# Kernel tuning notes

Measured on AMD Instinct MI355X. Metric: run time of the kernel, lower is better.

## Reference

```python
import jax, jax.numpy as jnp
import numpy as np

B, T, F, H = 256, 4096, 16, 64

def setup_inputs() -> dict:
    key = jax.random.key(0)
    ks = jax.random.split(key, 16)
    rn = lambda k, s, sc=0.1: jax.random.normal(k, s, dtype=jnp.float32) * sc
    return {
        'x':    rn(ks[0], (B, T, F), 1.0),
        'Wi1':  rn(ks[1], (F, 3 * H)), 'bi1': jnp.zeros((3 * H,), jnp.float32),
        'Whr1': rn(ks[2], (H, H)), 'Whz1': rn(ks[3], (H, H)), 'Whn1': rn(ks[4], (H, H)),
        'bhn1': jnp.zeros((H,), jnp.float32),
        'Wi2':  rn(ks[5], (H, 3 * H)), 'bi2': jnp.zeros((3 * H,), jnp.float32),
        'Whr2': rn(ks[6], (H, H)), 'Whz2': rn(ks[7], (H, H)), 'Whn2': rn(ks[8], (H, H)),
        'bhn2': jnp.zeros((H,), jnp.float32),
        'Wp':   rn(ks[9], (F, H)), 'bp': jnp.zeros((H,), jnp.float32),
        'Wa':   rn(ks[10], (H, 1)), 'ba': jnp.zeros((1,), jnp.float32),
        'W1':   rn(ks[11], (H, 128)), 'b1': jnp.zeros((128,), jnp.float32),
        'W2':   rn(ks[12], (128, 64)), 'b2': jnp.zeros((64,), jnp.float32),
        'W3':   rn(ks[13], (64, 32)), 'b3': jnp.zeros((32,), jnp.float32),
        'W4':   rn(ks[14], (32, 2)), 'b4': jnp.zeros((2,), jnp.float32),
    }

def gru_layer(x, Wi, bi, Whr, Whz, Whn, bhn):
    # flax GRUCell math: r/z hidden kernels bias-free; n hidden kernel has bias.
    b, h = x.shape[0], Whr.shape[0]
    xi = jnp.einsum('btf,fk->btk', x, Wi) + bi  # precompute input projections (B,T,3H)
    def step(hprev, xt):
        ir, iz, inn = jnp.split(xt, 3, axis=-1)
        r = jax.nn.sigmoid(ir + hprev @ Whr)
        z = jax.nn.sigmoid(iz + hprev @ Whz)
        n = jnp.tanh(inn + r * (hprev @ Whn + bhn))
        hnew = (1.0 - z) * n + z * hprev
        return hnew, hnew
    h0 = jnp.zeros((b, h), x.dtype)
    _, ys = jax.lax.scan(step, h0, jnp.swapaxes(xi, 0, 1))  # (T,B,H)
    return jnp.swapaxes(ys, 0, 1)  # (B,T,H)

def reference(x, Wi1, bi1, Whr1, Whz1, Whn1, bhn1,
              Wi2, bi2, Whr2, Whz2, Whn2, bhn2,
              Wp, bp, Wa, ba, W1, b1, W2, b2, W3, b3, W4, b4):
    o1 = gru_layer(x, Wi1, bi1, Whr1, Whz1, Whn1, bhn1)
    x_proj = jnp.einsum('btf,fh->bth', x, Wp) + bp  # F != H -> project
    o1 = o1 + 0.5 * x_proj
    o2 = gru_layer(o1, Wi2, bi2, Whr2, Whz2, Whn2, bhn2) + 0.5 * o1
    scores = jnp.einsum('bth,ho->bto', o2, Wa) + ba  # (B,T,1)
    w = jax.nn.softmax(scores, axis=1)
    attended = jnp.sum(o2 * w, axis=1)  # (B,H)
    h1 = jax.nn.relu(attended @ W1 + b1)
    h2 = jax.nn.relu(h1 @ W2 + b2)
    h3 = jax.nn.relu(h2 @ W3 + b3)
    return h3 @ W4 + b4  # (B,2)
```

## Files before the change

kernel.cpp:

```cpp
#include <hip/hip_runtime.h>


#define B_ 256
#define T_ 4096
#define F_ 16
#define H_ 64
#define L2E 1.4426950408889634f

typedef float v2f __attribute__((ext_vector_type(2)));

__device__ __forceinline__ float sigm(float x) {
    float e = __builtin_amdgcn_exp2f(-L2E * x);
    return __builtin_amdgcn_rcpf(1.0f + e);
}
__device__ __forceinline__ float tanh_(float x) {
    float e = __builtin_amdgcn_exp2f(2.0f * L2E * x);
    return 1.0f - 2.0f * __builtin_amdgcn_rcpf(1.0f + e);
}
__device__ __forceinline__ v2f fma2(v2f a, v2f b, v2f c) {
    return __builtin_elementwise_fma(a, b, c);
}

#define DPPADD(x, ctrl) \
    ((x) + __builtin_bit_cast(float, __builtin_amdgcn_update_dpp( \
        0, __builtin_bit_cast(int, (x)), (ctrl), 0xF, 0xF, true)))

__device__ __forceinline__ float qsum(float x) {
    float t = DPPADD(x, 0xB1);
    return DPPADD(t, 0x4E);
}
__device__ __forceinline__ float wred(float x) {
    x = DPPADD(x, 0x111);
    x = DPPADD(x, 0x112);
    x = DPPADD(x, 0x114);
    x = DPPADD(x, 0x118);
    x = DPPADD(x, 0x142);
    x = DPPADD(x, 0x143);
    return x;
}

__launch_bounds__(256, 1)
__global__ void solar_rnn(const float* __restrict__ x,
                          const float* __restrict__ Wi1, const float* __restrict__ bi1,
                          const float* __restrict__ Whr1, const float* __restrict__ Whz1,
                          const float* __restrict__ Whn1, const float* __restrict__ bhn1,
                          const float* __restrict__ Wi2, const float* __restrict__ bi2,
                          const float* __restrict__ Whr2, const float* __restrict__ Whz2,
                          const float* __restrict__ Whn2, const float* __restrict__ bhn2,
                          const float* __restrict__ Wp, const float* __restrict__ bp,
                          const float* __restrict__ Wa,
                          const float* __restrict__ W1, const float* __restrict__ b1,
                          const float* __restrict__ W2, const float* __restrict__ b2,
                          const float* __restrict__ W3, const float* __restrict__ b3,
                          const float* __restrict__ W4, const float* __restrict__ b4,
                          float* __restrict__ out)
{
    const int b   = blockIdx.x;
    const int tid = threadIdx.x;
    const int v   = tid >> 6;
    const int j   = tid & 63;
    const int o   = j >> 2;
    const int s   = j & 3;
    const int col = 16 * v + o;

    __shared__ __align__(16) float h1p[2][H_];
    __shared__ __align__(16) float h2p[2][H_];
    __shared__ __align__(16) float xbuf[2][256];
    __shared__ float spl[2][4];
    __shared__ float sm_a[128];
    __shared__ float sm_b[128];

    int hoff[4];
    #pragma unroll
    for (int q = 0; q < 4; ++q) hoff[q] = 16 * s + 4 * ((q + s) & 3);

    v2f wr1p[8], wz1p[8], wn1p[8];
    v2f wr2p[8], wz2p[8], wn2p[8];
    v2f u2rp[8], u2zp[8], u2np[8];
    #pragma unroll
    for (int q = 0; q < 4; ++q) {
        const int rb = hoff[q];
        #pragma unroll
        for (int e = 0; e < 2; ++e) {
            const int r0 = rb + 2 * e, r1 = r0 + 1;
            const int m = 2 * q + e;
            wr1p[m] = v2f{Whr1[r0 * H_ + col], Whr1[r1 * H_ + col]};
            wz1p[m] = v2f{Whz1[r0 * H_ + col], Whz1[r1 * H_ + col]};
            wn1p[m] = v2f{Whn1[r0 * H_ + col], Whn1[r1 * H_ + col]};
            wr2p[m] = v2f{Whr2[r0 * H_ + col], Whr2[r1 * H_ + col]};
            wz2p[m] = v2f{Whz2[r0 * H_ + col], Whz2[r1 * H_ + col]};
            wn2p[m] = v2f{Whn2[r0 * H_ + col], Whn2[r1 * H_ + col]};
            u2rp[m] = v2f{Wi2[r0 * 192 + col],       Wi2[r1 * 192 + col]};
            u2zp[m] = v2f{Wi2[r0 * 192 + 64 + col],  Wi2[r1 * 192 + 64 + col]};
            u2np[m] = v2f{Wi2[r0 * 192 + 128 + col], Wi2[r1 * 192 + 128 + col]};
        }
    }
    float x2r[4], x2z[4], x2n[4];
    #pragma unroll
    for (int kk = 0; kk < 4; ++kk) {
        const int row = 4 * s + kk;
        float ar = 0.f, az = 0.f, an = 0.f;
        for (int m = 0; m < H_; ++m) {
            const float wp = Wp[row * H_ + m];
            ar = fmaf(wp, Wi2[m * 192 + col],       ar);
            az = fmaf(wp, Wi2[m * 192 + 64 + col],  az);
            an = fmaf(wp, Wi2[m * 192 + 128 + col], an);
        }
        x2r[kk] = 0.5f * ar; x2z[kk] = 0.5f * az; x2n[kk] = 0.5f * an;
    }
    v2f w1rp[2], w1zp[2], w1np[2], wpvp[2], x2rp[2], x2zp[2], x2np[2];
    #pragma unroll
    for (int m = 0; m < 2; ++m) {
        const int r0 = 4 * s + 2 * m, r1 = r0 + 1;
        w1rp[m] = v2f{Wi1[r0 * 192 + col],       Wi1[r1 * 192 + col]};
        w1zp[m] = v2f{Wi1[r0 * 192 + 64 + col],  Wi1[r1 * 192 + 64 + col]};
        w1np[m] = v2f{Wi1[r0 * 192 + 128 + col], Wi1[r1 * 192 + 128 + col]};
        wpvp[m] = v2f{Wp[r0 * H_ + col],         Wp[r1 * H_ + col]};
        x2rp[m] = v2f{x2r[2 * m], x2r[2 * m + 1]};
        x2zp[m] = v2f{x2z[2 * m], x2z[2 * m + 1]};
        x2np[m] = v2f{x2n[2 * m], x2n[2 * m + 1]};
    }
    float cbr = 0.f, cbz = 0.f, cbn = 0.f;
    for (int m = 0; m < H_; ++m) {
        const float bpm = bp[m];
        cbr = fmaf(bpm, Wi2[m * 192 + col],       cbr);
        cbz = fmaf(bpm, Wi2[m * 192 + 64 + col],  cbz);
        cbn = fmaf(bpm, Wi2[m * 192 + 128 + col], cbn);
    }
    const float b1r = bi1[col], b1z = bi1[64 + col], b1n = bi1[128 + col], bh1o = bhn1[col];
    const float bb2r = bi2[col]       + 0.5f * cbr;
    const float bb2z = bi2[64 + col]  + 0.5f * cbz;
    const float bb2n = bi2[128 + col] + 0.5f * cbn;
    const float bh2o = bhn2[col];
    const float bpo  = bp[col], wao = Wa[col];

    if (tid < 64) { h1p[0][j] = 0.f; h1p[1][j] = 0.f; h2p[0][j] = 0.f; h2p[1][j] = 0.f; }
    if (tid < 8)  spl[tid >> 2][tid & 3] = 0.f;
    const float* xb = x + (size_t)b * T_ * F_;
    float4 xnext;
    if (tid < 64) {
        const float4* gx = (const float4*)xb;
        ((float4*)xbuf[0])[j] = gx[j];
        xnext = gx[64 + j];
    }
    __syncthreads();

    float h1 = 0.f, h2 = 0.f, o1p = 0.f, o2a = 0.f;
    float am = -3.0e38f, al = 0.f, aa = 0.f;
    v2f xprev0 = v2f{0.f, 0.f}, xprev1 = v2f{0.f, 0.f};

    #pragma unroll 1
    for (int t = 0; t < T_; ++t) {
        const int tb = t & 1;

        const float4 xt4 = ((const float4*)xbuf[(t >> 4) & 1])[(t & 15) * 4 + s];
        const float* h1r = h1p[tb ^ 1];
        const float* h2r = h2p[tb];
        v2f hv1[8], hv2[8];
        #pragma unroll
        for (int q = 0; q < 4; ++q) {
            const float4 a = *(const float4*)&h1r[hoff[q]];
            const float4 c = *(const float4*)&h2r[hoff[q]];
            hv1[2 * q]     = v2f{a.x, a.y};
            hv1[2 * q + 1] = v2f{a.z, a.w};
            hv2[2 * q]     = v2f{c.x, c.y};
            hv2[2 * q + 1] = v2f{c.z, c.w};
        }
        float gp = spl[tb][s];

        const v2f zz = v2f{0.f, 0.f};
        v2f Aar2 = fma2(x2rp[0], xprev0, fma2(x2rp[1], xprev1, zz));
        v2f Aaz2 = fma2(x2zp[0], xprev0, fma2(x2zp[1], xprev1, zz));
        v2f Aan2 = fma2(x2np[0], xprev0, fma2(x2np[1], xprev1, zz));
        const v2f xt0 = v2f{xt4.x, xt4.y}, xt1 = v2f{xt4.z, xt4.w};
        v2f Aar1 = fma2(w1rp[0], xt0, fma2(w1rp[1], xt1, zz));
        v2f Aaz1 = fma2(w1zp[0], xt0, fma2(w1zp[1], xt1, zz));
        v2f Aan1 = fma2(w1np[0], xt0, fma2(w1np[1], xt1, zz));
        v2f Aax1 = fma2(wpvp[0], xt0, fma2(wpvp[1], xt1, zz));
        v2f Ahn1 = zz, Ahn2 = zz;
        #pragma unroll
        for (int m = 0; m < 8; ++m) {
            Aar1 = fma2(hv1[m], wr1p[m], Aar1);
            Aaz1 = fma2(hv1[m], wz1p[m], Aaz1);
            Ahn1 = fma2(hv1[m], wn1p[m], Ahn1);
            Aar2 = fma2(hv1[m], u2rp[m], Aar2);
            Aaz2 = fma2(hv1[m], u2zp[m], Aaz2);
            Aan2 = fma2(hv1[m], u2np[m], Aan2);
            Aar2 = fma2(hv2[m], wr2p[m], Aar2);
            Aaz2 = fma2(hv2[m], wz2p[m], Aaz2);
            Ahn2 = fma2(hv2[m], wn2p[m], Ahn2);
        }
        const float g0 = qsum(Aar1.x + Aar1.y);
        const float g1 = qsum(Aaz1.x + Aaz1.y);
        const float g2 = qsum(Aan1.x + Aan1.y);
        const float g3 = qsum(Ahn1.x + Ahn1.y);
        const float g4 = qsum(Aax1.x + Aax1.y);
        const float g5 = qsum(Aan2.x + Aan2.y);
        const float g6 = qsum(Aar2.x + Aar2.y);
        const float g7 = qsum(Aaz2.x + Aaz2.y);
        const float g8 = qsum(Ahn2.x + Ahn2.y);
        gp = qsum(gp);

        if (t >= 2) {
            const float p  = 0.25f * gp;
            const float mn = fmaxf(am, p);
            const float ca = __builtin_amdgcn_exp2f((am - mn) * L2E);
            const float ce = __builtin_amdgcn_exp2f((p  - mn) * L2E);
            al = fmaf(al, ca, ce);
            aa = fmaf(aa, ca, ce * o2a);
            am = mn;
        }

        const float r2 = sigm(g6 + bb2r);
        const float z2 = sigm(g7 + bb2z);
        const float n2 = tanh_((g5 + bb2n) + r2 * (g8 + bh2o));
        h2 = n2 + z2 * (h2 - n2);
        h2 = (t == 0) ? 0.f : h2;
        const float o2 = h2 + 0.5f * o1p;
        float ps = wred(o2 * wao);
        if (j == 63) spl[tb ^ 1][v] = ps;
        if (s == 0) h2p[tb ^ 1][col] = h2;
        o2a = o2;

        const float r1 = sigm(g0 + b1r);
        const float z1 = sigm(g1 + b1z);
        const float n1 = tanh_((g2 + b1n) + r1 * (g3 + bh1o));
        h1 = n1 + z1 * (h1 - n1);
        o1p = h1 + 0.5f * (g4 + bpo);
        if (s == 0) h1p[tb][col] = h1;

        if ((t & 15) == 8 && tid < 64) {
            const int c = t >> 4;
            if (c + 1 < T_ / 16) {
                ((float4*)xbuf[(c + 1) & 1])[j] = xnext;
                if (c + 2 < T_ / 16) xnext = ((const float4*)xb)[(c + 2) * 64 + j];
            }
        }
        xprev0 = xt0; xprev1 = xt1;
        __syncthreads();
    }

    {
        const float* h1r = h1p[1];
        const float* h2r = h2p[0];
        v2f hv1[8], hv2[8];
        #pragma unroll
        for (int q = 0; q < 4; ++q) {
            const float4 a = *(const float4*)&h1r[hoff[q]];
            const float4 c = *(const float4*)&h2r[hoff[q]];
            hv1[2 * q]     = v2f{a.x, a.y};
            hv1[2 * q + 1] = v2f{a.z, a.w};
            hv2[2 * q]     = v2f{c.x, c.y};
            hv2[2 * q + 1] = v2f{c.z, c.w};
        }
        const v2f zz = v2f{0.f, 0.f};
        v2f Aar2 = fma2(x2rp[0], xprev0, fma2(x2rp[1], xprev1, zz));
        v2f Aaz2 = fma2(x2zp[0], xprev0, fma2(x2zp[1], xprev1, zz));
        v2f Aan2 = fma2(x2np[0], xprev0, fma2(x2np[1], xprev1, zz));
        v2f Ahn2 = zz;
        #pragma unroll
        for (int m = 0; m < 8; ++m) {
            Aar2 = fma2(hv1[m], u2rp[m], Aar2);
            Aaz2 = fma2(hv1[m], u2zp[m], Aaz2);
            Aan2 = fma2(hv1[m], u2np[m], Aan2);
            Aar2 = fma2(hv2[m], wr2p[m], Aar2);
            Aaz2 = fma2(hv2[m], wz2p[m], Aaz2);
            Ahn2 = fma2(hv2[m], wn2p[m], Ahn2);
        }
        const float g5 = qsum(Aan2.x + Aan2.y);
        const float g6 = qsum(Aar2.x + Aar2.y);
        const float g7 = qsum(Aaz2.x + Aaz2.y);
        const float g8 = qsum(Ahn2.x + Ahn2.y);
        float gp = qsum(spl[0][s]);
        {
            const float p  = 0.25f * gp;
            const float mn = fmaxf(am, p);
            const float ca = __builtin_amdgcn_exp2f((am - mn) * L2E);
            const float ce = __builtin_amdgcn_exp2f((p  - mn) * L2E);
            al = fmaf(al, ca, ce);
            aa = fmaf(aa, ca, ce * o2a);
            am = mn;
        }
        const float r2 = sigm(g6 + bb2r);
        const float z2 = sigm(g7 + bb2z);
        const float n2 = tanh_((g5 + bb2n) + r2 * (g8 + bh2o));
        h2 = n2 + z2 * (h2 - n2);
        const float o2 = h2 + 0.5f * o1p;
        float ps = wred(o2 * wao);
        if (j == 63) spl[1][v] = ps;
        __syncthreads();
        float gq = qsum(spl[1][s]);
        {
            const float p  = 0.25f * gq;
            const float mn = fmaxf(am, p);
            const float ca = __builtin_amdgcn_exp2f((am - mn) * L2E);
            const float ce = __builtin_amdgcn_exp2f((p  - mn) * L2E);
            al = fmaf(al, ca, ce);
            aa = fmaf(aa, ca, ce * o2);
            am = mn;
        }
    }

    if (s == 0) sm_a[col] = aa / al;
    __syncthreads();

    float v1 = 0.f;
    if (tid < 128) {
        float a = b1[tid];
        for (int k = 0; k < 64; ++k) a = fmaf(sm_a[k], W1[k * 128 + tid], a);
        v1 = fmaxf(a, 0.f);
    }
    __syncthreads();
    if (tid < 128) sm_b[tid] = v1;
    __syncthreads();
    if (tid < 64) {
        float a = b2[tid];
        for (int k = 0; k < 128; ++k) a = fmaf(sm_b[k], W2[k * 64 + tid], a);
        sm_a[tid] = fmaxf(a, 0.f);
    }
    __syncthreads();
    if (tid < 32) {
        float a = b3[tid];
        for (int k = 0; k < 64; ++k) a = fmaf(sm_a[k], W3[k * 32 + tid], a);
        sm_b[tid] = fmaxf(a, 0.f);
    }
    __syncthreads();
    if (tid < 2) {
        float a = b4[tid];
        for (int k = 0; k < 32; ++k) a = fmaf(sm_b[k], W4[k * 2 + tid], a);
        out[b * 2 + tid] = a;
    }
}

extern "C" void kernel_launch(void* const* d_in, const int* in_sizes, int n_in,
                              void* d_out, int out_size, void* d_ws, size_t ws_size,
                              hipStream_t stream) {
    const float* x    = (const float*)d_in[0];
    const float* Wi1  = (const float*)d_in[1];
    const float* bi1  = (const float*)d_in[2];
    const float* Whr1 = (const float*)d_in[3];
    const float* Whz1 = (const float*)d_in[4];
    const float* Whn1 = (const float*)d_in[5];
    const float* bhn1 = (const float*)d_in[6];
    const float* Wi2  = (const float*)d_in[7];
    const float* bi2  = (const float*)d_in[8];
    const float* Whr2 = (const float*)d_in[9];
    const float* Whz2 = (const float*)d_in[10];
    const float* Whn2 = (const float*)d_in[11];
    const float* bhn2 = (const float*)d_in[12];
    const float* Wp   = (const float*)d_in[13];
    const float* bp   = (const float*)d_in[14];
    const float* Wa   = (const float*)d_in[15];
    const float* W1   = (const float*)d_in[17];
    const float* b1   = (const float*)d_in[18];
    const float* W2   = (const float*)d_in[19];
    const float* b2   = (const float*)d_in[20];
    const float* W3   = (const float*)d_in[21];
    const float* b3   = (const float*)d_in[22];
    const float* W4   = (const float*)d_in[23];
    const float* b4   = (const float*)d_in[24];

    solar_rnn<<<dim3(B_), dim3(256), 0, stream>>>(
        x, Wi1, bi1, Whr1, Whz1, Whn1, bhn1,
        Wi2, bi2, Whr2, Whz2, Whn2, bhn2,
        Wp, bp, Wa, W1, b1, W2, b2, W3, b3, W4, b4,
        (float*)d_out);
}
```

Before: 2.619 ms.

## Split GRU layers across separate wavefront groups in a 512-thread block

Doubles the block to 512 threads and specialises waves: waves 0-3 run layer-1 GRU steps while waves 4-7 run the layer-2 step one timestep behind, exchanging h1 and o1 through shared memory. Each thread now holds only one layer's weights and does roughly half the per-step FMAs and reductions, cutting the serial per-step critical path. In exchange, every step's barrier now synchronises eight waves instead of four, and the two groups do unequal work per step (layer 2 does more FMAs).

```diff
diff --git a/kernel.cpp b/kernel.cpp
--- a/kernel.cpp
+++ b/kernel.cpp
@@ -39,7 +39,7 @@
     return x;
 }
 
-__launch_bounds__(256, 1)
+__launch_bounds__(512, 1)
 __global__ void solar_rnn(const float* __restrict__ x,
                           const float* __restrict__ Wi1, const float* __restrict__ bi1,
                           const float* __restrict__ Whr1, const float* __restrict__ Whz1,
@@ -57,14 +57,17 @@
 {
     const int b   = blockIdx.x;
     const int tid = threadIdx.x;
-    const int v   = tid >> 6;
+    const int w   = tid >> 6;
     const int j   = tid & 63;
+    const bool l2r = (w >= 4);
+    const int v   = w & 3;
     const int o   = j >> 2;
     const int s   = j & 3;
     const int col = 16 * v + o;
 
-    __shared__ __align__(16) float h1p[2][H_];
-    __shared__ __align__(16) float h2p[2][H_];
+    __shared__ float h1p[2][H_];
+    __shared__ float h2p[2][H_];
+    __shared__ float o1pl[2][H_];
     __shared__ __align__(16) float xbuf[2][256];
     __shared__ float spl[2][4];
     __shared__ float sm_a[128];
@@ -74,68 +77,85 @@
     #pragma unroll
     for (int q = 0; q < 4; ++q) hoff[q] = 16 * s + 4 * ((q + s) & 3);
 
-    v2f wr1p[8], wz1p[8], wn1p[8];
-    v2f wr2p[8], wz2p[8], wn2p[8];
-    v2f u2rp[8], u2zp[8], u2np[8];
-    #pragma unroll
-    for (int q = 0; q < 4; ++q) {
-        const int rb = hoff[q];
-        #pragma unroll
-        for (int e = 0; e < 2; ++e) {
-            const int r0 = rb + 2 * e, r1 = r0 + 1;
-            const int m = 2 * q + e;
-            wr1p[m] = v2f{Whr1[r0 * H_ + col], Whr1[r1 * H_ + col]};
-            wz1p[m] = v2f{Whz1[r0 * H_ + col], Whz1[r1 * H_ + col]};
-            wn1p[m] = v2f{Whn1[r0 * H_ + col], Whn1[r1 * H_ + col]};
-            wr2p[m] = v2f{Whr2[r0 * H_ + col], Whr2[r1 * H_ + col]};
-            wz2p[m] = v2f{Whz2[r0 * H_ + col], Whz2[r1 * H_ + col]};
-            wn2p[m] = v2f{Whn2[r0 * H_ + col], Whn2[r1 * H_ + col]};
-            u2rp[m] = v2f{Wi2[r0 * 192 + col],       Wi2[r1 * 192 + col]};
-            u2zp[m] = v2f{Wi2[r0 * 192 + 64 + col],  Wi2[r1 * 192 + 64 + col]};
-            u2np[m] = v2f{Wi2[r0 * 192 + 128 + col], Wi2[r1 * 192 + 128 + col]};
-        }
-    }
-    float x2r[4], x2z[4], x2n[4];
-    #pragma unroll
-    for (int kk = 0; kk < 4; ++kk) {
-        const int row = 4 * s + kk;
-        float ar = 0.f, az = 0.f, an = 0.f;
+    v2f hw0[8], hw1[8], hw2[8], hw3[8], hw4[8], hw5[8];
+    v2f xw0[2], xw1[2], xw2[2], xw3[2];
+    float c0, c1, c2, c3, c4;
+
+    if (!l2r) {
+        #pragma unroll
+        for (int q = 0; q < 4; ++q) {
+            const int rb = hoff[q];
+            #pragma unroll
+            for (int e = 0; e < 2; ++e) {
+                const int r0 = rb + 2 * e, r1 = r0 + 1, m = 2 * q + e;
+                hw0[m] = v2f{Whr1[r0 * H_ + col], Whr1[r1 * H_ + col]};
+                hw1[m] = v2f{Whz1[r0 * H_ + col], Whz1[r1 * H_ + col]};
+                hw2[m] = v2f{Whn1[r0 * H_ + col], Whn1[r1 * H_ + col]};
+            }
+        }
+        #pragma unroll
+        for (int m = 0; m < 2; ++m) {
+            const int r0 = 4 * s + 2 * m, r1 = r0 + 1;
+            xw0[m] = v2f{Wi1[r0 * 192 + col],       Wi1[r1 * 192 + col]};
+            xw1[m] = v2f{Wi1[r0 * 192 + 64 + col],  Wi1[r1 * 192 + 64 + col]};
+            xw2[m] = v2f{Wi1[r0 * 192 + 128 + col], Wi1[r1 * 192 + 128 + col]};
+            xw3[m] = v2f{Wp[r0 * H_ + col],         Wp[r1 * H_ + col]};
+        }
+        c0 = bi1[col]; c1 = bi1[64 + col]; c2 = bi1[128 + col];
+        c3 = bhn1[col]; c4 = bp[col];
+    } else {
+        #pragma unroll
+        for (int q = 0; q < 4; ++q) {
+            const int rb = hoff[q];
+            #pragma unroll
+            for (int e = 0; e < 2; ++e) {
+                const int r0 = rb + 2 * e, r1 = r0 + 1, m = 2 * q + e;
+                hw0[m] = v2f{Whr2[r0 * H_ + col], Whr2[r1 * H_ + col]};
+                hw1[m] = v2f{Whz2[r0 * H_ + col], Whz2[r1 * H_ + col]};
+                hw2[m] = v2f{Whn2[r0 * H_ + col], Whn2[r1 * H_ + col]};
+                hw3[m] = v2f{Wi2[r0 * 192 + col],       Wi2[r1 * 192 + col]};
+                hw4[m] = v2f{Wi2[r0 * 192 + 64 + col],  Wi2[r1 * 192 + 64 + col]};
+                hw5[m] = v2f{Wi2[r0 * 192 + 128 + col], Wi2[r1 * 192 + 128 + col]};
+            }
+        }
+        float x2r[4], x2z[4], x2n[4];
+        #pragma unroll
+        for (int kk = 0; kk < 4; ++kk) {
+            const int row = 4 * s + kk;
+            float ar = 0.f, az = 0.f, an = 0.f;
+            for (int m = 0; m < H_; ++m) {
+                const float wp = Wp[row * H_ + m];
+                ar = fmaf(wp, Wi2[m * 192 + col],       ar);
+                az = fmaf(wp, Wi2[m * 192 + 64 + col],  az);
+                an = fmaf(wp, Wi2[m * 192 + 128 + col], an);
+            }
+            x2r[kk] = 0.5f * ar; x2z[kk] = 0.5f * az; x2n[kk] = 0.5f * an;
+        }
+        #pragma unroll
+        for (int m = 0; m < 2; ++m) {
+            xw0[m] = v2f{x2r[2 * m], x2r[2 * m + 1]};
+            xw1[m] = v2f{x2z[2 * m], x2z[2 * m + 1]};
+            xw2[m] = v2f{x2n[2 * m], x2n[2 * m + 1]};
+        }
+        float cbr = 0.f, cbz = 0.f, cbn = 0.f;
         for (int m = 0; m < H_; ++m) {
-            const float wp = Wp[row * H_ + m];
-            ar = fmaf(wp, Wi2[m * 192 + col],       ar);
-            az = fmaf(wp, Wi2[m * 192 + 64 + col],  az);
-            an = fmaf(wp, Wi2[m * 192 + 128 + col], an);
-        }
-        x2r[kk] = 0.5f * ar; x2z[kk] = 0.5f * az; x2n[kk] = 0.5f * an;
-    }
-    v2f w1rp[2], w1zp[2], w1np[2], wpvp[2], x2rp[2], x2zp[2], x2np[2];
-    #pragma unroll
-    for (int m = 0; m < 2; ++m) {
-        const int r0 = 4 * s + 2 * m, r1 = r0 + 1;
-        w1rp[m] = v2f{Wi1[r0 * 192 + col],       Wi1[r1 * 192 + col]};
-        w1zp[m] = v2f{Wi1[r0 * 192 + 64 + col],  Wi1[r1 * 192 + 64 + col]};
-        w1np[m] = v2f{Wi1[r0 * 192 + 128 + col], Wi1[r1 * 192 + 128 + col]};
-        wpvp[m] = v2f{Wp[r0 * H_ + col],         Wp[r1 * H_ + col]};
-        x2rp[m] = v2f{x2r[2 * m], x2r[2 * m + 1]};
-        x2zp[m] = v2f{x2z[2 * m], x2z[2 * m + 1]};
-        x2np[m] = v2f{x2n[2 * m], x2n[2 * m + 1]};
-    }
-    float cbr = 0.f, cbz = 0.f, cbn = 0.f;
-    for (int m = 0; m < H_; ++m) {
-        const float bpm = bp[m];
-        cbr = fmaf(bpm, Wi2[m * 192 + col],       cbr);
-        cbz = fmaf(bpm, Wi2[m * 192 + 64 + col],  cbz);
-        cbn = fmaf(bpm, Wi2[m * 192 + 128 + col], cbn);
-    }
-    const float b1r = bi1[col], b1z = bi1[64 + col], b1n = bi1[128 + col], bh1o = bhn1[col];
-    const float bb2r = bi2[col]       + 0.5f * cbr;
-    const float bb2z = bi2[64 + col]  + 0.5f * cbz;
-    const float bb2n = bi2[128 + col] + 0.5f * cbn;
-    const float bh2o = bhn2[col];
-    const float bpo  = bp[col], wao = Wa[col];
-
-    if (tid < 64) { h1p[0][j] = 0.f; h1p[1][j] = 0.f; h2p[0][j] = 0.f; h2p[1][j] = 0.f; }
-    if (tid < 8)  spl[tid >> 2][tid & 3] = 0.f;
+            const float bpm = bp[m];
+            cbr = fmaf(bpm, Wi2[m * 192 + col],       cbr);
+            cbz = fmaf(bpm, Wi2[m * 192 + 64 + col],  cbz);
+            cbn = fmaf(bpm, Wi2[m * 192 + 128 + col], cbn);
+        }
+        c0 = bi2[col]       + 0.5f * cbr;
+        c1 = bi2[64 + col]  + 0.5f * cbz;
+        c2 = bi2[128 + col] + 0.5f * cbn;
+        c3 = bhn2[col]; c4 = Wa[col];
+    }
+
+    if (tid < 64) {
+        h1p[0][j] = 0.f; h1p[1][j] = 0.f;
+        h2p[0][j] = 0.f; h2p[1][j] = 0.f;
+        o1pl[0][j] = 0.f; o1pl[1][j] = 0.f;
+    }
+    if (tid < 8) spl[tid >> 2][tid & 3] = 0.f;
     const float* xb = x + (size_t)b * T_ * F_;
     float4 xnext;
     if (tid < 64) {
@@ -145,132 +165,153 @@
     }
     __syncthreads();
 
-    float h1 = 0.f, h2 = 0.f, o1p = 0.f, o2a = 0.f;
+    float hS = 0.f;
+    float o2a = 0.f;
     float am = -3.0e38f, al = 0.f, aa = 0.f;
-    v2f xprev0 = v2f{0.f, 0.f}, xprev1 = v2f{0.f, 0.f};
+    const v2f zz = v2f{0.f, 0.f};
 
     #pragma unroll 1
     for (int t = 0; t < T_; ++t) {
         const int tb = t & 1;
-
-        const float4 xt4 = ((const float4*)xbuf[(t >> 4) & 1])[(t & 15) * 4 + s];
-        const float* h1r = h1p[tb ^ 1];
-        const float* h2r = h2p[tb];
-        v2f hv1[8], hv2[8];
+        if (!l2r) {
+            const float4 xt4 = ((const float4*)xbuf[(t >> 4) & 1])[(t & 15) * 4 + s];
+            const float* h1r = h1p[tb ^ 1];
+            v2f hv[8];
+            #pragma unroll
+            for (int q = 0; q < 4; ++q) {
+                const float4 a = *(const float4*)&h1r[hoff[q]];
+                hv[2 * q]     = v2f{a.x, a.y};
+                hv[2 * q + 1] = v2f{a.z, a.w};
+            }
+            const v2f xt0 = v2f{xt4.x, xt4.y}, xt1 = v2f{xt4.z, xt4.w};
+            v2f Ar = fma2(xw0[0], xt0, fma2(xw0[1], xt1, zz));
+            v2f Az = fma2(xw1[0], xt0, fma2(xw1[1], xt1, zz));
+            v2f An = fma2(xw2[0], xt0, fma2(xw2[1], xt1, zz));
+            v2f Ax = fma2(xw3[0], xt0, fma2(xw3[1], xt1, zz));
+            v2f Ah = zz;
+            #pragma unroll
+            for (int m = 0; m < 8; ++m) {
+                Ar = fma2(hv[m], hw0[m], Ar);
+                Az = fma2(hv[m], hw1[m], Az);
+                Ah = fma2(hv[m], hw2[m], Ah);
+            }
+            const float g0 = qsum(Ar.x + Ar.y);
+            const float g1 = qsum(Az.x + Az.y);
+            const float g2 = qsum(An.x + An.y);
+            const float g3 = qsum(Ah.x + Ah.y);
+            const float g4 = qsum(Ax.x + Ax.y);
+            const float r1 = sigm(g0 + c0);
+            const float z1 = sigm(g1 + c1);
+            const float n1 = tanh_((g2 + c2) + r1 * (g3 + c3));
+            hS = n1 + z1 * (hS - n1);
+            const float o1 = hS + 0.5f * (g4 + c4);
+            if (s == 0) { h1p[tb][col] = hS; o1pl[tb][col] = o1; }
+            if ((t & 15) == 8 && w == 0) {
+                const int c = t >> 4;
+                if (c + 1 < T_ / 16) {
+                    ((float4*)xbuf[(c + 1) & 1])[j] = xnext;
+                    if (c + 2 < T_ / 16) xnext = ((const float4*)xb)[(c + 2) * 64 + j];
+                }
+            }
+        } else {
+            v2f xm0 = zz, xm1 = zz;
+            if (t >= 1) {
+                const int tm = t - 1;
+                const float4 xm4 = ((const float4*)xbuf[(tm >> 4) & 1])[(tm & 15) * 4 + s];
+                xm0 = v2f{xm4.x, xm4.y}; xm1 = v2f{xm4.z, xm4.w};
+            }
+            const float* h1r = h1p[tb ^ 1];
+            const float* h2r = h2p[tb];
+            v2f hv[8], gv[8];
+            #pragma unroll
+            for (int q = 0; q < 4; ++q) {
+                const float4 a = *(const float4*)&h1r[hoff[q]];
+                const float4 c = *(const float4*)&h2r[hoff[q]];
+                hv[2 * q]     = v2f{a.x, a.y};
+                hv[2 * q + 1] = v2f{a.z, a.w};
+                gv[2 * q]     = v2f{c.x, c.y};
+                gv[2 * q + 1] = v2f{c.z, c.w};
+            }
+            const float o1r = o1pl[tb ^ 1][col];
+            float gp = spl[tb][s];
+
+            v2f Ar = fma2(xw0[0], xm0, fma2(xw0[1], xm1, zz));
+            v2f Az = fma2(xw1[0], xm0, fma2(xw1[1], xm1, zz));
+            v2f An = fma2(xw2[0], xm0, fma2(xw2[1], xm1, zz));
+            v2f Ah = zz;
+            #pragma unroll
+            for (int m = 0; m < 8; ++m) {
+                Ar = fma2(gv[m], hw0[m], Ar);
+                Az = fma2(gv[m], hw1[m], Az);
+                Ah = fma2(gv[m], hw2[m], Ah);
+                Ar = fma2(hv[m], hw3[m], Ar);
+                Az = fma2(hv[m], hw4[m], Az);
+                An = fma2(hv[m], hw5[m], An);
+            }
+            const float g6 = qsum(Ar.x + Ar.y);
+            const float g7 = qsum(Az.x + Az.y);
+            const float g5 = qsum(An.x + An.y);
+            const float g8 = qsum(Ah.x + Ah.y);
+            gp = qsum(gp);
+
+            if (t >= 2) {
+                const float p  = 0.25f * gp;
+                const float mn = fmaxf(am, p);
+                const float ca = __builtin_amdgcn_exp2f((am - mn) * L2E);
+                const float ce = __builtin_amdgcn_exp2f((p  - mn) * L2E);
+                al = fmaf(al, ca, ce);
+                aa = fmaf(aa, ca, ce * o2a);
+                am = mn;
+            }
+
+            const float r2 = sigm(g6 + c0);
+            const float z2 = sigm(g7 + c1);
+            const float n2 = tanh_((g5 + c2) + r2 * (g8 + c3));
+            hS = n2 + z2 * (hS - n2);
+            hS = (t == 0) ? 0.f : hS;
+            const float o2 = hS + 0.5f * o1r;
+            float ps = wred(o2 * c4);
+            if (j == 63) spl[tb ^ 1][v] = ps;
+            if (s == 0) h2p[tb ^ 1][col] = hS;
+            o2a = o2;
+        }
+        __syncthreads();
+    }
+
+    if (l2r) {
+        const int tm = T_ - 1;
+        const float4 xm4 = ((const float4*)xbuf[(tm >> 4) & 1])[(tm & 15) * 4 + s];
+        const v2f xm0 = v2f{xm4.x, xm4.y}, xm1 = v2f{xm4.z, xm4.w};
+        const float* h1r = h1p[1];
+        const float* h2r = h2p[0];
+        v2f hv[8], gv[8];
         #pragma unroll
         for (int q = 0; q < 4; ++q) {
             const float4 a = *(const float4*)&h1r[hoff[q]];
             const float4 c = *(const float4*)&h2r[hoff[q]];
-            hv1[2 * q]     = v2f{a.x, a.y};
-            hv1[2 * q + 1] = v2f{a.z, a.w};
-            hv2[2 * q]     = v2f{c.x, c.y};
-            hv2[2 * q + 1] = v2f{c.z, c.w};
-        }
-        float gp = spl[tb][s];
-
-        const v2f zz = v2f{0.f, 0.f};
-        v2f Aar2 = fma2(x2rp[0], xprev0, fma2(x2rp[1], xprev1, zz));
-        v2f Aaz2 = fma2(x2zp[0], xprev0, fma2(x2zp[1], xprev1, zz));
-        v2f Aan2 = fma2(x2np[0], xprev0, fma2(x2np[1], xprev1, zz));
-        const v2f xt0 = v2f{xt4.x, xt4.y}, xt1 = v2f{xt4.z, xt4.w};
-        v2f Aar1 = fma2(w1rp[0], xt0, fma2(w1rp[1], xt1, zz));
-        v2f Aaz1 = fma2(w1zp[0], xt0, fma2(w1zp[1], xt1, zz));
-        v2f Aan1 = fma2(w1np[0], xt0, fma2(w1np[1], xt1, zz));
-        v2f Aax1 = fma2(wpvp[0], xt0, fma2(wpvp[1], xt1, zz));
-        v2f Ahn1 = zz, Ahn2 = zz;
+            hv[2 * q]     = v2f{a.x, a.y};
+            hv[2 * q + 1] = v2f{a.z, a.w};
+            gv[2 * q]     = v2f{c.x, c.y};
+            gv[2 * q + 1] = v2f{c.z, c.w};
+        }
+        const float o1r = o1pl[1][col];
+        v2f Ar = fma2(xw0[0], xm0, fma2(xw0[1], xm1, zz));
+        v2f Az = fma2(xw1[0], xm0, fma2(xw1[1], xm1, zz));
+        v2f An = fma2(xw2[0], xm0, fma2(xw2[1], xm1, zz));
+        v2f Ah = zz;
         #pragma unroll
         for (int m = 0; m < 8; ++m) {
-            Aar1 = fma2(hv1[m], wr1p[m], Aar1);
-            Aaz1 = fma2(hv1[m], wz1p[m], Aaz1);
-            Ahn1 = fma2(hv1[m], wn1p[m], Ahn1);
-            Aar2 = fma2(hv1[m], u2rp[m], Aar2);
-            Aaz2 = fma2(hv1[m], u2zp[m], Aaz2);
-            Aan2 = fma2(hv1[m], u2np[m], Aan2);
-            Aar2 = fma2(hv2[m], wr2p[m], Aar2);
-            Aaz2 = fma2(hv2[m], wz2p[m], Aaz2);
-            Ahn2 = fma2(hv2[m], wn2p[m], Ahn2);
-        }
-        const float g0 = qsum(Aar1.x + Aar1.y);
-        const float g1 = qsum(Aaz1.x + Aaz1.y);
-        const float g2 = qsum(Aan1.x + Aan1.y);
-        const float g3 = qsum(Ahn1.x + Ahn1.y);
-        const float g4 = qsum(Aax1.x + Aax1.y);
-        const float g5 = qsum(Aan2.x + Aan2.y);
-        const float g6 = qsum(Aar2.x + Aar2.y);
-        const float g7 = qsum(Aaz2.x + Aaz2.y);
-        const float g8 = qsum(Ahn2.x + Ahn2.y);
-        gp = qsum(gp);
-
-        if (t >= 2) {
-            const float p  = 0.25f * gp;
-            const float mn = fmaxf(am, p);
-            const float ca = __builtin_amdgcn_exp2f((am - mn) * L2E);
-            const float ce = __builtin_amdgcn_exp2f((p  - mn) * L2E);
-            al = fmaf(al, ca, ce);
-            aa = fmaf(aa, ca, ce * o2a);
-            am = mn;
-        }
-
-        const float r2 = sigm(g6 + bb2r);
-        const float z2 = sigm(g7 + bb2z);
-        const float n2 = tanh_((g5 + bb2n) + r2 * (g8 + bh2o));
-        h2 = n2 + z2 * (h2 - n2);
-        h2 = (t == 0) ? 0.f : h2;
-        const float o2 = h2 + 0.5f * o1p;
-        float ps = wred(o2 * wao);
-        if (j == 63) spl[tb ^ 1][v] = ps;
-        if (s == 0) h2p[tb ^ 1][col] = h2;
-        o2a = o2;
-
-        const float r1 = sigm(g0 + b1r);
-        const float z1 = sigm(g1 + b1z);
-        const float n1 = tanh_((g2 + b1n) + r1 * (g3 + bh1o));
-        h1 = n1 + z1 * (h1 - n1);
-        o1p = h1 + 0.5f * (g4 + bpo);
-        if (s == 0) h1p[tb][col] = h1;
-
-        if ((t & 15) == 8 && tid < 64) {
-            const int c = t >> 4;
-            if (c + 1 < T_ / 16) {
-                ((float4*)xbuf[(c + 1) & 1])[j] = xnext;
-                if (c + 2 < T_ / 16) xnext = ((const float4*)xb)[(c + 2) * 64 + j];
-            }
-        }
-        xprev0 = xt0; xprev1 = xt1;
-        __syncthreads();
-    }
-
-    {
-        const float* h1r = h1p[1];
-        const float* h2r = h2p[0];
-        v2f hv1[8], hv2[8];
-        #pragma unroll
-        for (int q = 0; q < 4; ++q) {
-            const float4 a = *(const float4*)&h1r[hoff[q]];
-            const float4 c = *(const float4*)&h2r[hoff[q]];
-            hv1[2 * q]     = v2f{a.x, a.y};
-            hv1[2 * q + 1] = v2f{a.z, a.w};
-            hv2[2 * q]     = v2f{c.x, c.y};
-            hv2[2 * q + 1] = v2f{c.z, c.w};
-        }
-        const v2f zz = v2f{0.f, 0.f};
-        v2f Aar2 = fma2(x2rp[0], xprev0, fma2(x2rp[1], xprev1, zz));
-        v2f Aaz2 = fma2(x2zp[0], xprev0, fma2(x2zp[1], xprev1, zz));
-        v2f Aan2 = fma2(x2np[0], xprev0, fma2(x2np[1], xprev1, zz));
-        v2f Ahn2 = zz;
-        #pragma unroll
-        for (int m = 0; m < 8; ++m) {
-            Aar2 = fma2(hv1[m], u2rp[m], Aar2);
-            Aaz2 = fma2(hv1[m], u2zp[m], Aaz2);
-            Aan2 = fma2(hv1[m], u2np[m], Aan2);
-            Aar2 = fma2(hv2[m], wr2p[m], Aar2);
-            Aaz2 = fma2(hv2[m], wz2p[m], Aaz2);
-            Ahn2 = fma2(hv2[m], wn2p[m], Ahn2);
-        }
-        const float g5 = qsum(Aan2.x + Aan2.y);
-        const float g6 = qsum(Aar2.x + Aar2.y);
-        const float g7 = qsum(Aaz2.x + Aaz2.y);
-        const float g8 = qsum(Ahn2.x + Ahn2.y);
+            Ar = fma2(gv[m], hw0[m], Ar);
+            Az = fma2(gv[m], hw1[m], Az);
+            Ah = fma2(gv[m], hw2[m], Ah);
+            Ar = fma2(hv[m], hw3[m], Ar);
+            Az = fma2(hv[m], hw4[m], Az);
+            An = fma2(hv[m], hw5[m], An);
+        }
+        const float g6 = qsum(Ar.x + Ar.y);
+        const float g7 = qsum(Az.x + Az.y);
+        const float g5 = qsum(An.x + An.y);
+        const float g8 = qsum(Ah.x + Ah.y);
         float gp = qsum(spl[0][s]);
         {
             const float p  = 0.25f * gp;
@@ -281,27 +322,26 @@
             aa = fmaf(aa, ca, ce * o2a);
             am = mn;
         }
-        const float r2 = sigm(g6 + bb2r);
-        const float z2 = sigm(g7 + bb2z);
-        const float n2 = tanh_((g5 + bb2n) + r2 * (g8 + bh2o));
-        h2 = n2 + z2 * (h2 - n2);
-        const float o2 = h2 + 0.5f * o1p;
-        float ps = wred(o2 * wao);
+        const float r2 = sigm(g6 + c0);
+        const float z2 = sigm(g7 + c1);
+        const float n2 = tanh_((g5 + c2) + r2 * (g8 + c3));
+        hS = n2 + z2 * (hS - n2);
+        const float o2 = hS + 0.5f * o1r;
+        float ps = wred(o2 * c4);
         if (j == 63) spl[1][v] = ps;
-        __syncthreads();
+        o2a = o2;
+    }
+    __syncthreads();
+    if (l2r) {
         float gq = qsum(spl[1][s]);
-        {
-            const float p  = 0.25f * gq;
-            const float mn = fmaxf(am, p);
-            const float ca = __builtin_amdgcn_exp2f((am - mn) * L2E);
-            const float ce = __builtin_amdgcn_exp2f((p  - mn) * L2E);
-            al = fmaf(al, ca, ce);
-            aa = fmaf(aa, ca, ce * o2);
-            am = mn;
-        }
-    }
-
-    if (s == 0) sm_a[col] = aa / al;
+        const float p  = 0.25f * gq;
+        const float mn = fmaxf(am, p);
+        const float ca = __builtin_amdgcn_exp2f((am - mn) * L2E);
+        const float ce = __builtin_amdgcn_exp2f((p  - mn) * L2E);
+        al = fmaf(al, ca, ce);
+        aa = fmaf(aa, ca, ce * o2a);
+        if (s == 0) sm_a[col] = aa / al;
+    }
     __syncthreads();
 
     float v1 = 0.f;
@@ -360,7 +400,7 @@
     const float* W4   = (const float*)d_in[23];
     const float* b4   = (const float*)d_in[24];
 
-    solar_rnn<<<dim3(B_), dim3(256), 0, stream>>>(
+    solar_rnn<<<dim3(B_), dim3(512), 0, stream>>>(
         x, Wi1, bi1, Whr1, Whz1, Whn1, bhn1,
         Wi2, bi2, Whr2, Whz2, Whn2, bhn2,
         Wp, bp, Wa, W1, b1, W2, b2, W3, b3, W4, b4,
```

Result: faster. 2.420 ms (-7.6%).
